# Optimization experiments

Measured on AMD Instinct MI355X. Metric: run time of the kernel, lower is better.

The kernel has to match this reference:

```python
import jax, jax.numpy as jnp
import numpy as np

NEG = -9e9  # large negative used by the original torch code for masking


def setup_inputs() -> dict:
    key = jax.random.key(0)
    k1, k2, k3, k4 = jax.random.split(key, 4)
    B, N, L, D = 64, 128, 64, 768
    return {
        "text_embeddings": jax.random.normal(k1, (B, N, D), dtype=jnp.float32),
        "image_embeddings": jax.random.normal(k2, (B, L, D), dtype=jnp.float32),
        "text_mask": jax.random.randint(k3, (B, N), 0, 2, dtype=jnp.int32),
        "image_mask": jax.random.randint(k4, (B, L), 0, 2, dtype=jnp.int32),
    }


def _grounding(text_emb, image_emb, text_mask, image_mask):
    # Vectorized version of the B x B python loop in score_grounding.
    tm = text_mask.astype(text_emb.dtype)   # [B, N]
    im = image_mask.astype(text_emb.dtype)  # [B, L]
    # pairwise mask: mask[i, j, n, l] = text_mask[i, n] * image_mask[j, l]
    mask = tm[:, None, :, None] * im[None, :, None, :]            # [B, B, N, L]
    att = jnp.einsum('ind,jld->ijnl', text_emb, image_emb) * mask  # [B, B, N, L]
    att = jnp.where(att * mask != 0, att, NEG)
    # softmax over image spans (last dim), masked
    aw_first = jax.nn.softmax(att, axis=-1) * mask
    score1 = (aw_first * att).sum(-1).mean(-1)                     # [B, B]
    # softmax over text spans (dim 2 == the N axis), masked (transpose trick in torch)
    aw_second = jax.nn.softmax(att, axis=2) * mask
    score2 = (aw_second * att).sum(-1).mean(-1)                    # [B, B]
    sent_scores = score1 + score2                                  # [B, B]
    B = text_emb.shape[0]
    idx = jnp.arange(B)
    token_scores = att[idx, idx]                                   # diagonal pairs, [B, N, L]
    return sent_scores, token_scores


def reference(text_embeddings, image_embeddings, text_mask, image_mask):
    B = text_embeddings.shape[0]
    S, token_scores = _grounding(text_embeddings, image_embeddings, text_mask, image_mask)
    # text_emb_i2s = softmax(att_weights) @ image_emb
    text_emb_i2s = jnp.einsum('bnl,bld->bnd', jax.nn.softmax(token_scores, axis=-1), image_embeddings)
    # loss = -(sum diag logsoftmax(S, dim=1) + sum diag logsoftmax(S.T, dim=1)) / n
    ls1 = jnp.diagonal(jax.nn.log_softmax(S, axis=1))
    ls2 = jnp.diagonal(jax.nn.log_softmax(S.T, axis=1))
    loss = -(jnp.sum(ls1) + jnp.sum(ls2)) / B
    return loss, text_emb_i2s
```

## Files before the change

### kernel.cpp

```cpp
#include <hip/hip_runtime.h>
#include <math.h>

#define BSZ 64
#define NN  128
#define LL  64
#define DD  768
#define NEGV (-9e9f)

#define TQ (BSZ * NN * DD / 4)
#define IQ (BSZ * LL * DD / 4)

typedef _Float16 f16x8 __attribute__((ext_vector_type(8)));
typedef __attribute__((ext_vector_type(4))) float f32x4;

__device__ __forceinline__ void gl_lds16(const void* g, void* l) {
    __builtin_amdgcn_global_load_lds(
        (const __attribute__((address_space(1))) void*)g,
        (__attribute__((address_space(3))) void*)l, 16, 0, 0);
}

__global__ __launch_bounds__(256) void k_prep(
    const float4* __restrict__ t4, const float4* __restrict__ g4,
    ushort4* __restrict__ A, ushort4* __restrict__ B)
{
    int id = blockIdx.x * 256 + threadIdx.x;
    const float4* src; ushort4* dst; int idx;
    if (id < TQ) { src = t4; dst = A; idx = id; }
    else         { src = g4; dst = B; idx = id - TQ; }
    float4 x = src[idx];
    _Float16 h0 = (_Float16)x.x, h1 = (_Float16)x.y;
    _Float16 h2 = (_Float16)x.z, h3 = (_Float16)x.w;
    ushort4 o;
    o.x = __builtin_bit_cast(unsigned short, h0);
    o.y = __builtin_bit_cast(unsigned short, h1);
    o.z = __builtin_bit_cast(unsigned short, h2);
    o.w = __builtin_bit_cast(unsigned short, h3);
    dst[idx] = o;
}

__device__ __forceinline__ void stage_chunk(
    const unsigned short* __restrict__ pa, const unsigned short* __restrict__ pb,
    int k0, char* buf, int wave, int lane)
{
    int k8s = lane & 3;
#pragma unroll
    for (int c = 0; c < 2; c++) {
        int r  = c * 64 + wave * 16 + (lane >> 2);
        int k8 = k8s ^ ((r >> 1) & 3);
        gl_lds16(pa + (size_t)r * DD + k0 + k8 * 8, buf + c * 4096 + wave * 1024);
        gl_lds16(pb + (size_t)r * DD + k0 + k8 * 8, buf + 8192 + c * 4096 + wave * 1024);
    }
}

__global__ __launch_bounds__(256, 3) void k_scores(
    const unsigned short* __restrict__ A, const unsigned short* __restrict__ B,
    const int* __restrict__ tmask, const int* __restrict__ imask,
    float* __restrict__ S, float* __restrict__ W)
{
    __shared__ __align__(16) char stage[2][16384];
    __shared__ float tmi[NN];
    __shared__ float imj[NN];
    __shared__ float rowredL[NN][2];
    __shared__ float cpmax[2][NN];
    __shared__ float cpes[2][NN];
    __shared__ float cpws[2][NN];

    const int bid = blockIdx.x;
    const int grp = bid >> 4, idx = bid & 15;
    const int gi = grp >> 3, gj = grp & 7;
    const int i  = gi * 4 + (idx >> 2);
    const int jp = gj * 4 + (idx & 3);
    const int j0 = jp * 2;

    const int tid  = threadIdx.x;
    const int wave = tid >> 6;
    const int lane = tid & 63;
    const int quad = lane >> 4;
    const int l15  = lane & 15;
    const int wr   = wave & 1;
    const int wc   = wave >> 1;

    if (tid < NN) {
        tmi[tid] = tmask[i * NN + tid] ? 1.f : 0.f;
        imj[tid] = imask[j0 * LL + tid] ? 1.f : 0.f;
    }

    const unsigned short* pa = A + (size_t)i * NN * DD;
    const unsigned short* pb = B + (size_t)j0 * LL * DD;

    f32x4 acc[4][4];
    const f32x4 zf = {0.f, 0.f, 0.f, 0.f};
#pragma unroll
    for (int tr = 0; tr < 4; tr++)
#pragma unroll
        for (int tc = 0; tc < 4; tc++) acc[tr][tc] = zf;

    stage_chunk(pa, pb, 0, stage[0], wave, lane);
    __syncthreads();

    for (int c = 0; c < 24; c++) {
        if (c + 1 < 24)
            stage_chunk(pa, pb, (c + 1) << 5, stage[(c + 1) & 1], wave, lane);
        const char* Ab = stage[c & 1];
        const char* Bb = Ab + 8192;
        f16x8 af[4], bfr[4];
#pragma unroll
        for (int t = 0; t < 4; t++) {
            int row = wr * 64 + t * 16 + l15;
            af[t]  = *(const f16x8*)(Ab + ((row << 2) + (quad ^ ((row >> 1) & 3))) * 16);
            int col = wc * 64 + t * 16 + l15;
            bfr[t] = *(const f16x8*)(Bb + ((col << 2) + (quad ^ ((col >> 1) & 3))) * 16);
        }
#pragma unroll
        for (int tr = 0; tr < 4; tr++)
#pragma unroll
            for (int tc = 0; tc < 4; tc++)
                acc[tr][tc] = __builtin_amdgcn_mfma_f32_16x16x32_f16(
                    af[tr], bfr[tc], acc[tr][tc], 0, 0, 0);
        __syncthreads();
    }

    float tmr[4][4];
    float imc[4];
#pragma unroll
    for (int tr = 0; tr < 4; tr++)
#pragma unroll
        for (int rr = 0; rr < 4; rr++)
            tmr[tr][rr] = tmi[wr * 64 + tr * 16 + quad * 4 + rr];
#pragma unroll
    for (int tc = 0; tc < 4; tc++)
        imc[tc] = imj[wc * 64 + tc * 16 + l15];

    const bool wdiag = (jp == (i >> 1)) && (wc == (i & 1));

#pragma unroll
    for (int tr = 0; tr < 4; tr++) {
#pragma unroll
        for (int rr = 0; rr < 4; rr++) {
            int row = wr * 64 + tr * 16 + quad * 4 + rr;
            float tm = tmr[tr][rr];
            float vmv[4];
            float m = -INFINITY;
#pragma unroll
            for (int tc = 0; tc < 4; tc++) {
                float v = acc[tr][tc][rr];
                float vm = (tm != 0.f && imc[tc] != 0.f && v != 0.f) ? v : NEGV;
                vmv[tc] = vm;
                m = fmaxf(m, vm);
            }
            m = fmaxf(m, __shfl_xor(m, 1));
            m = fmaxf(m, __shfl_xor(m, 2));
            m = fmaxf(m, __shfl_xor(m, 4));
            m = fmaxf(m, __shfl_xor(m, 8));
            float ss = 0.f, ws = 0.f;
#pragma unroll
            for (int tc = 0; tc < 4; tc++) {
                float e = __expf(vmv[tc] - m);
                ss += e;
                ws += imc[tc] * e * vmv[tc];
            }
            ss += __shfl_xor(ss, 1); ss += __shfl_xor(ss, 2);
            ss += __shfl_xor(ss, 4); ss += __shfl_xor(ss, 8);
            ws += __shfl_xor(ws, 1); ws += __shfl_xor(ws, 2);
            ws += __shfl_xor(ws, 4); ws += __shfl_xor(ws, 8);
            if (l15 == 0) rowredL[row][wc] = tm * (ws / ss);
            if (wdiag) {
                float inv = 1.f / ss;
                float* Wb = W + (size_t)i * LL * NN;
#pragma unroll
                for (int tc = 0; tc < 4; tc++)
                    Wb[(size_t)(tc * 16 + l15) * NN + row] = __expf(vmv[tc] - m) * inv;
            }
        }
    }

#pragma unroll
    for (int tc = 0; tc < 4; tc++) {
        int col = wc * 64 + tc * 16 + l15;
        float cm = -INFINITY;
#pragma unroll
        for (int tr = 0; tr < 4; tr++)
#pragma unroll
            for (int rr = 0; rr < 4; rr++) {
                float v = acc[tr][tc][rr];
                float vm = (tmr[tr][rr] != 0.f && imc[tc] != 0.f && v != 0.f) ? v : NEGV;
                cm = fmaxf(cm, vm);
            }
        cm = fmaxf(cm, __shfl_xor(cm, 16));
        cm = fmaxf(cm, __shfl_xor(cm, 32));
        if (quad == 0) cpmax[wr][col] = cm;
    }
    __syncthreads();

#pragma unroll
    for (int tc = 0; tc < 4; tc++) {
        int col = wc * 64 + tc * 16 + l15;
        float m2 = fmaxf(cpmax[0][col], cpmax[1][col]);
        float es = 0.f, ws = 0.f;
#pragma unroll
        for (int tr = 0; tr < 4; tr++)
#pragma unroll
            for (int rr = 0; rr < 4; rr++) {
                float v = acc[tr][tc][rr];
                float tm = tmr[tr][rr];
                float vm = (tm != 0.f && imc[tc] != 0.f && v != 0.f) ? v : NEGV;
                float e = __expf(vm - m2);
                es += e;
                ws += tm * e * vm;
            }
        es += __shfl_xor(es, 16); es += __shfl_xor(es, 32);
        ws += __shfl_xor(ws, 16); ws += __shfl_xor(ws, 32);
        if (quad == 0) { cpes[wr][col] = es; cpws[wr][col] = ws; }
    }
    __syncthreads();

    if (wave < 2) {
        int jl = wave;
        float p = rowredL[lane][jl] + rowredL[64 + lane][jl];
        int col = jl * 64 + lane;
        float es = cpes[0][col] + cpes[1][col];
        float ws = cpws[0][col] + cpws[1][col];
        p += imj[col] * (ws / es);
#pragma unroll
        for (int off = 32; off; off >>= 1) p += __shfl_down(p, off);
        if (lane == 0) S[i * BSZ + j0 + jl] = p * (1.f / 128.f);
    }
}

__global__ __launch_bounds__(256) void k_i2s(
    const float* __restrict__ W, const float* __restrict__ img,
    float* __restrict__ out)
{
    __shared__ float Ws[LL * NN];
    const int b = blockIdx.x, tid = threadIdx.x;
    const float* Wb = W + (size_t)b * LL * NN;
#pragma unroll
    for (int q = 0; q < 8; q++) {
        int o = (tid + q * 256) * 4;
        *(float4*)&Ws[o] = *(const float4*)&Wb[o];
    }
    __syncthreads();

    const int d = blockIdx.y * 256 + tid;
    const float* ib = img + (size_t)b * LL * DD + d;
    float* ob = out + 1 + (size_t)b * NN * DD + d;

    for (int ng = 0; ng < 8; ng++) {
        float acc[16];
#pragma unroll
        for (int q = 0; q < 16; q++) acc[q] = 0.f;
        for (int l = 0; l < LL; l++) {
            float g = ib[(size_t)l * DD];
            const float* wrow = &Ws[l * NN + ng * 16];
            float4 w0 = *(const float4*)(wrow);
            float4 w1 = *(const float4*)(wrow + 4);
            float4 w2 = *(const float4*)(wrow + 8);
            float4 w3 = *(const float4*)(wrow + 12);
            acc[0]  = fmaf(w0.x, g, acc[0]);  acc[1]  = fmaf(w0.y, g, acc[1]);
            acc[2]  = fmaf(w0.z, g, acc[2]);  acc[3]  = fmaf(w0.w, g, acc[3]);
            acc[4]  = fmaf(w1.x, g, acc[4]);  acc[5]  = fmaf(w1.y, g, acc[5]);
            acc[6]  = fmaf(w1.z, g, acc[6]);  acc[7]  = fmaf(w1.w, g, acc[7]);
            acc[8]  = fmaf(w2.x, g, acc[8]);  acc[9]  = fmaf(w2.y, g, acc[9]);
            acc[10] = fmaf(w2.z, g, acc[10]); acc[11] = fmaf(w2.w, g, acc[11]);
            acc[12] = fmaf(w3.x, g, acc[12]); acc[13] = fmaf(w3.y, g, acc[13]);
            acc[14] = fmaf(w3.z, g, acc[14]); acc[15] = fmaf(w3.w, g, acc[15]);
        }
#pragma unroll
        for (int q = 0; q < 16; q++)
            ob[(size_t)(ng * 16 + q) * DD] = acc[q];
    }
}

__global__ __launch_bounds__(256) void k_loss(
    const float* __restrict__ S, float* __restrict__ out)
{
    __shared__ float Ss[BSZ * BSZ];
    const int tid = threadIdx.x;
#pragma unroll
    for (int q = 0; q < 16; q++) Ss[tid + q * 256] = S[tid + q * 256];
    __syncthreads();
    if (tid < 64) {
        float diag = Ss[tid * BSZ + tid];
        float m1 = -INFINITY, m2 = -INFINITY;
        for (int jj = 0; jj < BSZ; jj++) {
            m1 = fmaxf(m1, Ss[tid * BSZ + jj]);
            m2 = fmaxf(m2, Ss[jj * BSZ + tid]);
        }
        float s1 = 0.f, s2 = 0.f;
        for (int jj = 0; jj < BSZ; jj++) {
            s1 += __expf(Ss[tid * BSZ + jj] - m1);
            s2 += __expf(Ss[jj * BSZ + tid] - m2);
        }
        float p = 2.f * diag - (m1 + logf(s1)) - (m2 + logf(s2));
#pragma unroll
        for (int off = 32; off; off >>= 1) p += __shfl_down(p, off);
        if (tid == 0) out[0] = -p / (float)BSZ;
    }
}

extern "C" void kernel_launch(void* const* d_in, const int* in_sizes, int n_in,
                              void* d_out, int out_size, void* d_ws, size_t ws_size,
                              hipStream_t stream)
{
    (void)in_sizes; (void)n_in; (void)out_size; (void)ws_size;
    const float* text = (const float*)d_in[0];
    const float* img  = (const float*)d_in[1];
    const int*   tm   = (const int*)d_in[2];
    const int*   im   = (const int*)d_in[3];
    float* out = (float*)d_out;

    char* ws = (char*)d_ws;
    unsigned short* A = (unsigned short*)(ws);
    unsigned short* B = (unsigned short*)(ws + 12582912);
    float* S = (float*)(ws + 18874368);
    float* W = (float*)(ws + 18890752);

    k_prep<<<(TQ + IQ) / 256, 256, 0, stream>>>(
        (const float4*)text, (const float4*)img, (ushort4*)A, (ushort4*)B);

    k_scores<<<2048, 256, 0, stream>>>(A, B, tm, im, S, W);

    dim3 g2(BSZ, 3);
    k_i2s<<<g2, 256, 0, stream>>>(W, img, out);

    k_loss<<<1, 256, 0, stream>>>(S, out);
}
```

Baseline: 210.3 us.

## Restructure score kernel: stage full image tile in LDS, one wave per text pair

The score kernel now has each 512-thread block load one image batch's full 64x768 fp16 tile into LDS once. Each of the 8 waves handles a different text batch i, streaming its A rows directly from global memory with register prefetch. The column softmax across the two 64-row halves is merged online, which removes the cross-wave LDS reductions and extra barriers. The loss computation is folded into the i2s kernel to drop one launch. The 96KB+ LDS per block limits occupancy, and A operands are read from global without LDS reuse.

```diff
diff --git a/kernel.cpp b/kernel.cpp
--- a/kernel.cpp
+++ b/kernel.cpp
@@ -12,12 +12,6 @@
 
 typedef _Float16 f16x8 __attribute__((ext_vector_type(8)));
 typedef __attribute__((ext_vector_type(4))) float f32x4;
-
-__device__ __forceinline__ void gl_lds16(const void* g, void* l) {
-    __builtin_amdgcn_global_load_lds(
-        (const __attribute__((address_space(1))) void*)g,
-        (__attribute__((address_space(3))) void*)l, 16, 0, 0);
-}
 
 __global__ __launch_bounds__(256) void k_prep(
     const float4* __restrict__ t4, const float4* __restrict__ g4,
@@ -38,206 +32,217 @@
     dst[idx] = o;
 }
 
-__device__ __forceinline__ void stage_chunk(
-    const unsigned short* __restrict__ pa, const unsigned short* __restrict__ pb,
-    int k0, char* buf, int wave, int lane)
-{
-    int k8s = lane & 3;
-#pragma unroll
-    for (int c = 0; c < 2; c++) {
-        int r  = c * 64 + wave * 16 + (lane >> 2);
-        int k8 = k8s ^ ((r >> 1) & 3);
-        gl_lds16(pa + (size_t)r * DD + k0 + k8 * 8, buf + c * 4096 + wave * 1024);
-        gl_lds16(pb + (size_t)r * DD + k0 + k8 * 8, buf + 8192 + c * 4096 + wave * 1024);
-    }
-}
-
-__global__ __launch_bounds__(256, 3) void k_scores(
+__global__ __launch_bounds__(512, 2) void k_scores(
     const unsigned short* __restrict__ A, const unsigned short* __restrict__ B,
     const int* __restrict__ tmask, const int* __restrict__ imask,
     float* __restrict__ S, float* __restrict__ W)
 {
-    __shared__ __align__(16) char stage[2][16384];
-    __shared__ float tmi[NN];
-    __shared__ float imj[NN];
-    __shared__ float rowredL[NN][2];
-    __shared__ float cpmax[2][NN];
-    __shared__ float cpes[2][NN];
-    __shared__ float cpws[2][NN];
+    __shared__ __align__(16) char Bs[24 * 4096];
+    __shared__ float tmiS[8 * NN];
+    __shared__ float imjS[LL];
 
     const int bid = blockIdx.x;
-    const int grp = bid >> 4, idx = bid & 15;
-    const int gi = grp >> 3, gj = grp & 7;
-    const int i  = gi * 4 + (idx >> 2);
-    const int jp = gj * 4 + (idx & 3);
-    const int j0 = jp * 2;
+    const int j  = bid >> 3;
+    const int ig = bid & 7;
 
     const int tid  = threadIdx.x;
     const int wave = tid >> 6;
     const int lane = tid & 63;
     const int quad = lane >> 4;
     const int l15  = lane & 15;
-    const int wr   = wave & 1;
-    const int wc   = wave >> 1;
-
-    if (tid < NN) {
-        tmi[tid] = tmask[i * NN + tid] ? 1.f : 0.f;
-        imj[tid] = imask[j0 * LL + tid] ? 1.f : 0.f;
-    }
-
-    const unsigned short* pa = A + (size_t)i * NN * DD;
-    const unsigned short* pb = B + (size_t)j0 * LL * DD;
-
-    f32x4 acc[4][4];
-    const f32x4 zf = {0.f, 0.f, 0.f, 0.f};
-#pragma unroll
-    for (int tr = 0; tr < 4; tr++)
-#pragma unroll
-        for (int tc = 0; tc < 4; tc++) acc[tr][tc] = zf;
-
-    stage_chunk(pa, pb, 0, stage[0], wave, lane);
+
+    {
+        const unsigned short* pb = B + (size_t)j * LL * DD;
+#pragma unroll
+        for (int it = 0; it < 12; it++) {
+            int idx = it * 512 + tid;
+            int c   = idx >> 8;
+            int r   = idx & 255;
+            int col = r >> 2, k8 = r & 3;
+            float4 v = *(const float4*)(pb + (size_t)col * DD + c * 32 + k8 * 8);
+            int slot = (col << 2) + (k8 ^ ((col >> 1) & 3));
+            *(float4*)(Bs + c * 4096 + slot * 16) = v;
+        }
+        for (int it = tid; it < 8 * NN; it += 512) {
+            int il = it >> 7, n = it & 127;
+            tmiS[it] = tmask[(ig * 8 + il) * NN + n] ? 1.f : 0.f;
+        }
+        if (tid < LL) imjS[tid] = imask[j * LL + tid] ? 1.f : 0.f;
+    }
     __syncthreads();
 
-    for (int c = 0; c < 24; c++) {
-        if (c + 1 < 24)
-            stage_chunk(pa, pb, (c + 1) << 5, stage[(c + 1) & 1], wave, lane);
-        const char* Ab = stage[c & 1];
-        const char* Bb = Ab + 8192;
-        f16x8 af[4], bfr[4];
-#pragma unroll
-        for (int t = 0; t < 4; t++) {
-            int row = wr * 64 + t * 16 + l15;
-            af[t]  = *(const f16x8*)(Ab + ((row << 2) + (quad ^ ((row >> 1) & 3))) * 16);
-            int col = wc * 64 + t * 16 + l15;
-            bfr[t] = *(const f16x8*)(Bb + ((col << 2) + (quad ^ ((col >> 1) & 3))) * 16);
-        }
+    const int i = ig * 8 + wave;
+    const bool diag = (j == i);
+    float* Wb = W + (size_t)i * LL * NN;
+
+    float imc[4];
+#pragma unroll
+    for (int tc = 0; tc < 4; tc++) imc[tc] = imjS[tc * 16 + l15];
+
+    float rowacc = 0.f;
+    float Mc[4], Ec[4], Wc[4];
+
+#pragma unroll
+    for (int half = 0; half < 2; half++) {
+        float tmr[4][4];
 #pragma unroll
         for (int tr = 0; tr < 4; tr++)
 #pragma unroll
-            for (int tc = 0; tc < 4; tc++)
-                acc[tr][tc] = __builtin_amdgcn_mfma_f32_16x16x32_f16(
-                    af[tr], bfr[tc], acc[tr][tc], 0, 0, 0);
-        __syncthreads();
-    }
-
-    float tmr[4][4];
-    float imc[4];
-#pragma unroll
-    for (int tr = 0; tr < 4; tr++)
-#pragma unroll
-        for (int rr = 0; rr < 4; rr++)
-            tmr[tr][rr] = tmi[wr * 64 + tr * 16 + quad * 4 + rr];
+            for (int rr = 0; rr < 4; rr++)
+                tmr[tr][rr] = tmiS[wave * NN + half * 64 + tr * 16 + quad * 4 + rr];
+
+        const unsigned short* pA =
+            A + ((size_t)(i * NN + half * 64) * DD);
+
+        f32x4 acc[4][4];
+        const f32x4 zf = {0.f, 0.f, 0.f, 0.f};
+#pragma unroll
+        for (int tr = 0; tr < 4; tr++)
+#pragma unroll
+            for (int tc = 0; tc < 4; tc++) acc[tr][tc] = zf;
+
+        f16x8 afc[4], afn[4];
+#pragma unroll
+        for (int tr = 0; tr < 4; tr++)
+            afc[tr] = *(const f16x8*)(pA + (size_t)(tr * 16 + l15) * DD + quad * 8);
+#pragma unroll
+        for (int c = 0; c < 24; c++) {
+            if (c < 23) {
+#pragma unroll
+                for (int tr = 0; tr < 4; tr++)
+                    afn[tr] = *(const f16x8*)(pA + (size_t)(tr * 16 + l15) * DD
+                                              + (c + 1) * 32 + quad * 8);
+            }
+            f16x8 bf[4];
+#pragma unroll
+            for (int tc = 0; tc < 4; tc++) {
+                int col = tc * 16 + l15;
+                bf[tc] = *(const f16x8*)(Bs + c * 4096 +
+                         ((col << 2) + (quad ^ ((col >> 1) & 3))) * 16);
+            }
+#pragma unroll
+            for (int tr = 0; tr < 4; tr++)
+#pragma unroll
+                for (int tc = 0; tc < 4; tc++)
+                    acc[tr][tc] = __builtin_amdgcn_mfma_f32_16x16x32_f16(
+                        afc[tr], bf[tc], acc[tr][tc], 0, 0, 0);
+            if (c < 23) {
+#pragma unroll
+                for (int tr = 0; tr < 4; tr++) afc[tr] = afn[tr];
+            }
+        }
+
+#pragma unroll
+        for (int tr = 0; tr < 4; tr++) {
+#pragma unroll
+            for (int rr = 0; rr < 4; rr++) {
+                int row = half * 64 + tr * 16 + quad * 4 + rr;
+                float tm = tmr[tr][rr];
+                float vmv[4];
+                float m = -INFINITY;
+#pragma unroll
+                for (int tc = 0; tc < 4; tc++) {
+                    float v = acc[tr][tc][rr];
+                    float vm = (tm != 0.f && imc[tc] != 0.f && v != 0.f) ? v : NEGV;
+                    vmv[tc] = vm;
+                    m = fmaxf(m, vm);
+                }
+                m = fmaxf(m, __shfl_xor(m, 1));
+                m = fmaxf(m, __shfl_xor(m, 2));
+                m = fmaxf(m, __shfl_xor(m, 4));
+                m = fmaxf(m, __shfl_xor(m, 8));
+                float ss = 0.f, ws = 0.f;
+#pragma unroll
+                for (int tc = 0; tc < 4; tc++) {
+                    float e = __expf(vmv[tc] - m);
+                    ss += e;
+                    ws += imc[tc] * e * vmv[tc];
+                }
+                ss += __shfl_xor(ss, 1); ss += __shfl_xor(ss, 2);
+                ss += __shfl_xor(ss, 4); ss += __shfl_xor(ss, 8);
+                ws += __shfl_xor(ws, 1); ws += __shfl_xor(ws, 2);
+                ws += __shfl_xor(ws, 4); ws += __shfl_xor(ws, 8);
+                if (l15 == 0) rowacc += tm * (ws / ss);
+                if (diag) {
+                    float inv = 1.f / ss;
+#pragma unroll
+                    for (int tc = 0; tc < 4; tc++)
+                        Wb[(size_t)(tc * 16 + l15) * NN + row] =
+                            __expf(vmv[tc] - m) * inv;
+                }
+            }
+        }
+
+#pragma unroll
+        for (int tc = 0; tc < 4; tc++) {
+            float ic = imc[tc];
+            float cm = -INFINITY;
+#pragma unroll
+            for (int tr = 0; tr < 4; tr++)
+#pragma unroll
+                for (int rr = 0; rr < 4; rr++) {
+                    float v = acc[tr][tc][rr];
+                    float tm = tmr[tr][rr];
+                    float vm = (tm != 0.f && ic != 0.f && v != 0.f) ? v : NEGV;
+                    cm = fmaxf(cm, vm);
+                }
+            cm = fmaxf(cm, __shfl_xor(cm, 16));
+            cm = fmaxf(cm, __shfl_xor(cm, 32));
+            float es = 0.f, wsum = 0.f;
+#pragma unroll
+            for (int tr = 0; tr < 4; tr++)
+#pragma unroll
+                for (int rr = 0; rr < 4; rr++) {
+                    float v = acc[tr][tc][rr];
+                    float tm = tmr[tr][rr];
+                    float vm = (tm != 0.f && ic != 0.f && v != 0.f) ? v : NEGV;
+                    float e = __expf(vm - cm);
+                    es += e;
+                    wsum += tm * e * vm;
+                }
+            es += __shfl_xor(es, 16); es += __shfl_xor(es, 32);
+            wsum += __shfl_xor(wsum, 16); wsum += __shfl_xor(wsum, 32);
+            if (half == 0) { Mc[tc] = cm; Ec[tc] = es; Wc[tc] = wsum; }
+            else {
+                float mn = fmaxf(Mc[tc], cm);
+                float a = __expf(Mc[tc] - mn), b = __expf(cm - mn);
+                Ec[tc] = Ec[tc] * a + es * b;
+                Wc[tc] = Wc[tc] * a + wsum * b;
+                Mc[tc] = mn;
+            }
+        }
+    }
+
+    float colsum = 0.f;
 #pragma unroll
     for (int tc = 0; tc < 4; tc++)
-        imc[tc] = imj[wc * 64 + tc * 16 + l15];
-
-    const bool wdiag = (jp == (i >> 1)) && (wc == (i & 1));
-
-#pragma unroll
-    for (int tr = 0; tr < 4; tr++) {
-#pragma unroll
-        for (int rr = 0; rr < 4; rr++) {
-            int row = wr * 64 + tr * 16 + quad * 4 + rr;
-            float tm = tmr[tr][rr];
-            float vmv[4];
-            float m = -INFINITY;
-#pragma unroll
-            for (int tc = 0; tc < 4; tc++) {
-                float v = acc[tr][tc][rr];
-                float vm = (tm != 0.f && imc[tc] != 0.f && v != 0.f) ? v : NEGV;
-                vmv[tc] = vm;
-                m = fmaxf(m, vm);
-            }
-            m = fmaxf(m, __shfl_xor(m, 1));
-            m = fmaxf(m, __shfl_xor(m, 2));
-            m = fmaxf(m, __shfl_xor(m, 4));
-            m = fmaxf(m, __shfl_xor(m, 8));
-            float ss = 0.f, ws = 0.f;
-#pragma unroll
-            for (int tc = 0; tc < 4; tc++) {
-                float e = __expf(vmv[tc] - m);
-                ss += e;
-                ws += imc[tc] * e * vmv[tc];
-            }
-            ss += __shfl_xor(ss, 1); ss += __shfl_xor(ss, 2);
-            ss += __shfl_xor(ss, 4); ss += __shfl_xor(ss, 8);
-            ws += __shfl_xor(ws, 1); ws += __shfl_xor(ws, 2);
-            ws += __shfl_xor(ws, 4); ws += __shfl_xor(ws, 8);
-            if (l15 == 0) rowredL[row][wc] = tm * (ws / ss);
-            if (wdiag) {
-                float inv = 1.f / ss;
-                float* Wb = W + (size_t)i * LL * NN;
-#pragma unroll
-                for (int tc = 0; tc < 4; tc++)
-                    Wb[(size_t)(tc * 16 + l15) * NN + row] = __expf(vmv[tc] - m) * inv;
-            }
-        }
-    }
-
-#pragma unroll
-    for (int tc = 0; tc < 4; tc++) {
-        int col = wc * 64 + tc * 16 + l15;
-        float cm = -INFINITY;
-#pragma unroll
-        for (int tr = 0; tr < 4; tr++)
-#pragma unroll
-            for (int rr = 0; rr < 4; rr++) {
-                float v = acc[tr][tc][rr];
-                float vm = (tmr[tr][rr] != 0.f && imc[tc] != 0.f && v != 0.f) ? v : NEGV;
-                cm = fmaxf(cm, vm);
-            }
-        cm = fmaxf(cm, __shfl_xor(cm, 16));
-        cm = fmaxf(cm, __shfl_xor(cm, 32));
-        if (quad == 0) cpmax[wr][col] = cm;
-    }
-    __syncthreads();
-
-#pragma unroll
-    for (int tc = 0; tc < 4; tc++) {
-        int col = wc * 64 + tc * 16 + l15;
-        float m2 = fmaxf(cpmax[0][col], cpmax[1][col]);
-        float es = 0.f, ws = 0.f;
-#pragma unroll
-        for (int tr = 0; tr < 4; tr++)
-#pragma unroll
-            for (int rr = 0; rr < 4; rr++) {
-                float v = acc[tr][tc][rr];
-                float tm = tmr[tr][rr];
-                float vm = (tm != 0.f && imc[tc] != 0.f && v != 0.f) ? v : NEGV;
-                float e = __expf(vm - m2);
-                es += e;
-                ws += tm * e * vm;
-            }
-        es += __shfl_xor(es, 16); es += __shfl_xor(es, 32);
-        ws += __shfl_xor(ws, 16); ws += __shfl_xor(ws, 32);
-        if (quad == 0) { cpes[wr][col] = es; cpws[wr][col] = ws; }
-    }
-    __syncthreads();
-
-    if (wave < 2) {
-        int jl = wave;
-        float p = rowredL[lane][jl] + rowredL[64 + lane][jl];
-        int col = jl * 64 + lane;
-        float es = cpes[0][col] + cpes[1][col];
-        float ws = cpws[0][col] + cpws[1][col];
-        p += imj[col] * (ws / es);
-#pragma unroll
-        for (int off = 32; off; off >>= 1) p += __shfl_down(p, off);
-        if (lane == 0) S[i * BSZ + j0 + jl] = p * (1.f / 128.f);
-    }
+        colsum += imc[tc] * (Wc[tc] / Ec[tc]);
+    colsum += __shfl_xor(colsum, 1); colsum += __shfl_xor(colsum, 2);
+    colsum += __shfl_xor(colsum, 4); colsum += __shfl_xor(colsum, 8);
+    float rt = rowacc;
+    rt += __shfl_xor(rt, 1);  rt += __shfl_xor(rt, 2);
+    rt += __shfl_xor(rt, 4);  rt += __shfl_xor(rt, 8);
+    rt += __shfl_xor(rt, 16); rt += __shfl_xor(rt, 32);
+    if (lane == 0) S[i * BSZ + j] = (rt + colsum) * (1.f / 128.f);
 }
 
 __global__ __launch_bounds__(256) void k_i2s(
     const float* __restrict__ W, const float* __restrict__ img,
-    float* __restrict__ out)
+    const float* __restrict__ S, float* __restrict__ out)
 {
     __shared__ float Ws[LL * NN];
+    __shared__ float Ss[BSZ * BSZ];
     const int b = blockIdx.x, tid = threadIdx.x;
     const float* Wb = W + (size_t)b * LL * NN;
 #pragma unroll
     for (int q = 0; q < 8; q++) {
         int o = (tid + q * 256) * 4;
         *(float4*)&Ws[o] = *(const float4*)&Wb[o];
+    }
+    const bool doloss = (blockIdx.x == 0 && blockIdx.y == 0);
+    if (doloss) {
+#pragma unroll
+        for (int q = 0; q < 16; q++) Ss[tid + q * 256] = S[tid + q * 256];
     }
     __syncthreads();
 
@@ -269,17 +274,8 @@
         for (int q = 0; q < 16; q++)
             ob[(size_t)(ng * 16 + q) * DD] = acc[q];
     }
-}
-
-__global__ __launch_bounds__(256) void k_loss(
-    const float* __restrict__ S, float* __restrict__ out)
-{
-    __shared__ float Ss[BSZ * BSZ];
-    const int tid = threadIdx.x;
-#pragma unroll
-    for (int q = 0; q < 16; q++) Ss[tid + q * 256] = S[tid + q * 256];
-    __syncthreads();
-    if (tid < 64) {
+
+    if (doloss && tid < 64) {
         float diag = Ss[tid * BSZ + tid];
         float m1 = -INFINITY, m2 = -INFINITY;
         for (int jj = 0; jj < BSZ; jj++) {
@@ -318,10 +314,8 @@
     k_prep<<<(TQ + IQ) / 256, 256, 0, stream>>>(
         (const float4*)text, (const float4*)img, (ushort4*)A, (ushort4*)B);
 
-    k_scores<<<2048, 256, 0, stream>>>(A, B, tm, im, S, W);
+    k_scores<<<512, 512, 0, stream>>>(A, B, tm, im, S, W);
 
     dim3 g2(BSZ, 3);
-    k_i2s<<<g2, 256, 0, stream>>>(W, img, out);
-
-    k_loss<<<1, 256, 0, stream>>>(S, out);
+    k_i2s<<<g2, 256, 0, stream>>>(W, img, S, out);
 }
```

After: 307.1 us. 1.46x slower.
